# Optimization experiments

Measured on AMD Instinct MI355X. Metric: run time of the kernel, lower is better.

Reference implementation:

```python
import jax, jax.numpy as jnp
import numpy as np

N_NODES = 100000
N_EDGES = 6400000
IN_CH = 128
HID = 32
OUT = 16


def setup_inputs() -> dict:
    key = jax.random.key(0)
    k1, k2, k3, k4 = jax.random.split(key, 4)
    x = jax.random.normal(k1, (N_NODES, IN_CH), dtype=jnp.float32)
    edge_index = jax.random.randint(k2, (2, N_EDGES), 0, N_NODES, dtype=jnp.int64)
    # Glorot-style init like PyG GCNConv
    W1 = jax.random.normal(k3, (IN_CH, HID), dtype=jnp.float32) * (1.0 / np.sqrt(IN_CH))
    b1 = jnp.zeros((HID,), dtype=jnp.float32)
    W2 = jax.random.normal(k4, (HID, OUT), dtype=jnp.float32) * (1.0 / np.sqrt(HID))
    b2 = jnp.zeros((OUT,), dtype=jnp.float32)
    return {"x": x, "edge_index": edge_index, "W1": W1, "b1": b1, "W2": W2, "b2": b2}


def _gcn_layer(h, W, b, row, col, norm, n_nodes):
    # transform then propagate (PyG GCNConv order)
    m = h @ W                                   # [N, F_out]
    msg = m[row] * norm[:, None]                # gather + scale, [E+N, F_out]
    agg = jax.ops.segment_sum(msg, col, num_segments=n_nodes)
    return agg + b


def reference(x, edge_index, W1, b1, W2, b2):
    n = x.shape[0]
    loops = jnp.arange(n, dtype=edge_index.dtype)
    row = jnp.concatenate([edge_index[0], loops])  # source
    col = jnp.concatenate([edge_index[1], loops])  # target (aggregation index)
    # symmetric GCN normalization with self-loops; deg >= 1 always
    deg = jax.ops.segment_sum(jnp.ones_like(col, dtype=x.dtype), col, num_segments=n)
    deg_inv_sqrt = jax.lax.rsqrt(deg)
    norm = deg_inv_sqrt[row] * deg_inv_sqrt[col]
    h = jax.nn.relu(_gcn_layer(x, W1, b1, row, col, norm, n))
    # dropout p=0.5 is identity in eval mode
    return _gcn_layer(h, W2, b2, row, col, norm, n)
```

## Files before the change

### kernel.cpp

```cpp
#include <hip/hip_runtime.h>
#include <hip/hip_bf16.h>

#define IN_CH 128
#define HID 32
#define OUT_CH 16
#define NPW 128
#define NPW_SHIFT 7
#define NB_MAX 1024
#define FB_GRID 256
#define FB_THREADS 1024
#define CAP 12288
#define SCAN_CHUNK 1024
#define NXCD 8
#define EPT 8

typedef int vint4 __attribute__((ext_vector_type(4)));
typedef vint4 vint4u __attribute__((aligned(4)));

__global__ void detect_dtype(const void* ei, long long ecount, int n, int* flag) {
    int lane = threadIdx.x;
    const long long* p = (const long long*)ei;
    long long st = ecount / 64; if (st < 1) st = 1;
    long long idx = (long long)lane * st;
    bool ok = true;
    if (idx < ecount) {
        long long v = p[idx];
        ok = (v >= 0 && v < n);
    }
    unsigned long long mask = __ballot(ok);
    if (lane == 0) *flag = (mask == ~0ULL) ? 1 : 0;
}

__device__ __forceinline__ int load_idx(const void* ei, long long i, int is64) {
    return is64 ? (int)((const long long*)ei)[i] : ((const int*)ei)[i];
}

__device__ __forceinline__ void load_idx8_nt(const void* ei, long long off, int is64,
                                             int* c) {
    if (is64) {
        const long long* p = (const long long*)ei + off;
#pragma unroll
        for (int j = 0; j < 8; ++j) c[j] = (int)__builtin_nontemporal_load(p + j);
    } else {
        vint4 v0 = __builtin_nontemporal_load((const vint4*)((const int*)ei + off));
        vint4 v1 = __builtin_nontemporal_load((const vint4*)((const int*)ei + off + 4));
        c[0] = v0.x; c[1] = v0.y; c[2] = v0.z; c[3] = v0.w;
        c[4] = v1.x; c[5] = v1.y; c[6] = v1.z; c[7] = v1.w;
    }
}

__device__ __forceinline__ float bf_lo(unsigned int u) { return __uint_as_float(u << 16); }
__device__ __forceinline__ float bf_hi(unsigned int u) { return __uint_as_float(u & 0xFFFF0000u); }

__global__ __launch_bounds__(256) void zero_int(int* p, int n) {
    int i = blockIdx.x * 256 + threadIdx.x;
    if (i < n) p[i] = 0;
}

__global__ __launch_bounds__(256) void zero_float(float* p, long long n) {
    long long i = (long long)blockIdx.x * 256 + threadIdx.x;
    if (i < n) p[i] = 0.f;
}

__global__ __launch_bounds__(FB_THREADS) void bucket_hist(const void* ei, long long E,
                                                          const int* flag, int* bhist,
                                                          int nb, long long chunk) {
    __shared__ int hist[NB_MAX];
    for (int i = threadIdx.x; i < nb; i += FB_THREADS) hist[i] = 0;
    __syncthreads();
    long long lo = (long long)blockIdx.x * chunk;
    long long hi = lo + chunk; if (hi > E) hi = E;
    int is64 = *flag;
    if ((E & 7) == 0) {
        for (long long e = lo + (long long)threadIdx.x * EPT; e + EPT <= hi;
             e += (long long)FB_THREADS * EPT) {
            int c[8]; load_idx8_nt(ei, E + e, is64, c);
#pragma unroll
            for (int j = 0; j < 8; ++j) atomicAdd(&hist[c[j] >> NPW_SHIFT], 1);
        }
    } else {
        for (long long e = lo + threadIdx.x; e < hi; e += FB_THREADS)
            atomicAdd(&hist[load_idx(ei, E + e, is64) >> NPW_SHIFT], 1);
    }
    __syncthreads();
    for (int b = threadIdx.x; b < nb; b += FB_THREADS)
        bhist[b * FB_GRID + blockIdx.x] = hist[b];
}

__global__ __launch_bounds__(256) void scan_blocks(int* bhist, int* btot, int nb) {
    __shared__ int sd[FB_GRID];
    int b = blockIdx.x, t = threadIdx.x;
    int* p = bhist + (long long)b * FB_GRID;
    int v = p[t];
    sd[t] = v; __syncthreads();
    for (int off = 1; off < FB_GRID; off <<= 1) {
        int u = (t >= off) ? sd[t - off] : 0;
        __syncthreads(); sd[t] += u; __syncthreads();
    }
    p[t] = sd[t] - v;
    if (t == FB_GRID - 1) btot[b] = sd[t];
}

__global__ __launch_bounds__(1024) void scan_buckets(const int* btot, int* bstart, int nb) {
    __shared__ int sd[1024];
    int t = threadIdx.x;
    int a0 = (2 * t < nb) ? btot[2 * t] : 0;
    int a1 = (2 * t + 1 < nb) ? btot[2 * t + 1] : 0;
    sd[t] = a0 + a1; __syncthreads();
    for (int off = 1; off < 1024; off <<= 1) {
        int v = (t >= off) ? sd[t - off] : 0;
        __syncthreads(); sd[t] += v; __syncthreads();
    }
    int excl = sd[t] - (a0 + a1);
    if (2 * t < nb)     bstart[2 * t] = excl;
    if (2 * t + 1 < nb) bstart[2 * t + 1] = excl + a0;
    if (t == 1023) bstart[nb] = sd[t];
}

__global__ __launch_bounds__(FB_THREADS) void fill_bucket(const void* ei, long long E,
                                                          const int* flag,
                                                          const int* bhist,
                                                          const int* bstart,
                                                          int* bucketed, int nb,
                                                          long long chunk) {
    __shared__ int cur[NB_MAX];
    for (int b = threadIdx.x; b < nb; b += FB_THREADS)
        cur[b] = bstart[b] + bhist[b * FB_GRID + blockIdx.x];
    __syncthreads();
    long long lo = (long long)blockIdx.x * chunk;
    long long hi = lo + chunk; if (hi > E) hi = E;
    int is64 = *flag;
    if ((E & 7) == 0) {
        for (long long e = lo + (long long)threadIdx.x * EPT; e + EPT <= hi;
             e += (long long)FB_THREADS * EPT) {
            int c[8], r[8];
            load_idx8_nt(ei, E + e, is64, c);
            load_idx8_nt(ei, e, is64, r);
#pragma unroll
            for (int j = 0; j < 8; ++j) {
                int b = c[j] >> NPW_SHIFT;
                int pos = atomicAdd(&cur[b], 1);
                bucketed[pos] = r[j] | ((c[j] & (NPW - 1)) << 17);
            }
        }
    } else {
        for (long long e = lo + threadIdx.x; e < hi; e += FB_THREADS) {
            int col = load_idx(ei, E + e, is64);
            int row = load_idx(ei, e, is64);
            int b = col >> NPW_SHIFT;
            int pos = atomicAdd(&cur[b], 1);
            bucketed[pos] = row | ((col & (NPW - 1)) << 17);
        }
    }
}

__global__ __launch_bounds__(512) void csr_sort(const int* __restrict__ bucketed,
                                                const int* __restrict__ bstart,
                                                int* __restrict__ csr,
                                                int* __restrict__ offs,
                                                float* __restrict__ dinv,
                                                int nb, int n) {
    __shared__ int lds_e[CAP];
    __shared__ int hist[NPW];
    __shared__ int cur[NPW];
    int b = blockIdx.x, t = threadIdx.x;
    int s0 = bstart[b], s1 = bstart[b + 1];
    int cnt = s1 - s0;
    if (t < NPW) hist[t] = 0;
    __syncthreads();
    bool fit = (cnt <= CAP);
    int cnt4 = cnt & ~3;
    if (fit) {
        for (int i = t * 4; i < cnt4; i += 2048) {
            vint4u e4 = *(const vint4u*)(bucketed + s0 + i);
            lds_e[i + 0] = e4.x; atomicAdd(&hist[e4.x >> 17], 1);
            lds_e[i + 1] = e4.y; atomicAdd(&hist[e4.y >> 17], 1);
            lds_e[i + 2] = e4.z; atomicAdd(&hist[e4.z >> 17], 1);
            lds_e[i + 3] = e4.w; atomicAdd(&hist[e4.w >> 17], 1);
        }
        for (int i = cnt4 + t; i < cnt; i += 512) {
            int e = bucketed[s0 + i];
            lds_e[i] = e;
            atomicAdd(&hist[e >> 17], 1);
        }
    } else {
        for (int i = t * 4; i < cnt4; i += 2048) {
            vint4u e4 = *(const vint4u*)(bucketed + s0 + i);
            atomicAdd(&hist[e4.x >> 17], 1);
            atomicAdd(&hist[e4.y >> 17], 1);
            atomicAdd(&hist[e4.z >> 17], 1);
            atomicAdd(&hist[e4.w >> 17], 1);
        }
        for (int i = cnt4 + t; i < cnt; i += 512)
            atomicAdd(&hist[bucketed[s0 + i] >> 17], 1);
    }
    __syncthreads();
    if (t == 0) {
        int run = 0;
        for (int k = 0; k < NPW; ++k) { cur[k] = run; run += hist[k]; }
    }
    __syncthreads();
    if (t < NPW) {
        int node = b * NPW + t;
        if (node < n) {
            offs[node] = s0 + cur[t];
            dinv[node] = 1.0f / sqrtf((float)(hist[t] + 1));
        }
    }
    if (b == nb - 1 && t == 0) offs[n] = s1;
    __syncthreads();
    if (fit) {
        for (int i = t; i < cnt; i += 512) {
            int e = lds_e[i];
            int pos = atomicAdd(&cur[e >> 17], 1);
            csr[s0 + pos] = e & 0x1FFFF;
        }
    } else {
        for (int i = t; i < cnt; i += 512) {
            int e = bucketed[s0 + i];
            int pos = atomicAdd(&cur[e >> 17], 1);
            csr[s0 + pos] = e & 0x1FFFF;
        }
    }
}

template <int BF16>
__global__ __launch_bounds__(256) void gemm1p(const float* __restrict__ x,
                                              const float* __restrict__ W1,
                                              const float* __restrict__ dinv,
                                              float* __restrict__ m1f,
                                              __hip_bfloat16* __restrict__ m1b, int n) {
    __shared__ float sW[IN_CH * HID];
    __shared__ float sx[8][IN_CH];
    for (int i = threadIdx.x; i < IN_CH * HID; i += 256) sW[i] = W1[i];
    int g = threadIdx.x >> 5;
    int c = threadIdx.x & 31;
    long long node = (long long)blockIdx.x * 8 + g;
    bool active = node < n;
    if (active) {
        const float4* xr = (const float4*)(x + node * IN_CH);
        float4 v = xr[c];
        sx[g][c * 4 + 0] = v.x; sx[g][c * 4 + 1] = v.y;
        sx[g][c * 4 + 2] = v.z; sx[g][c * 4 + 3] = v.w;
    }
    __syncthreads();
    if (!active) return;
    float acc = 0.f;
#pragma unroll
    for (int k = 0; k < IN_CH; ++k)
        acc = fmaf(sx[g][k], sW[k * HID + c], acc);
    float v = acc * dinv[node];
    if (BF16) m1b[(node << 5) + c] = __float2bfloat16(v);
    else      m1f[(node << 5) + c] = v;
}

template <int BF16>
__global__ __launch_bounds__(256) void gemm2p(const float* __restrict__ h,
                                              const float* __restrict__ W2,
                                              const float* __restrict__ dinv,
                                              float* __restrict__ m2f,
                                              __hip_bfloat16* __restrict__ m2b, int n) {
    __shared__ float sW[HID * OUT_CH];
    for (int i = threadIdx.x; i < HID * OUT_CH; i += 256) sW[i] = W2[i];
    __syncthreads();
    long long t = (long long)blockIdx.x * 256 + threadIdx.x;
    long long node = t >> 4;
    int c = (int)(t & 15);
    if (node >= n) return;
    const float* hr = h + node * HID;
    float acc = 0.f;
#pragma unroll
    for (int k = 0; k < HID; ++k)
        acc = fmaf(hr[k], sW[k * OUT_CH + c], acc);
    float v = acc * dinv[node];
    if (BF16) m2b[(node << 4) + c] = __float2bfloat16(v);
    else      m2f[(node << 4) + c] = v;
}

__global__ __launch_bounds__(256) void agg1_bf(const unsigned int* __restrict__ m1b,
                                               const int* __restrict__ csr,
                                               const int* __restrict__ offs,
                                               const float* __restrict__ dinv,
                                               const float* __restrict__ b1,
                                               float* __restrict__ h, int n) {
    int g = threadIdx.x >> 4;
    int c = threadIdx.x & 15;
    long long node = (long long)blockIdx.x * 16 + g;
    if (node >= n) return;
    unsigned int us = m1b[(node << 4) + c];
    float accL = bf_lo(us), accH = bf_hi(us);
    int s = offs[node], e1 = offs[node + 1];
    for (; s + 7 < e1; s += 8) {
        vint4u a = *(const vint4u*)(csr + s);
        vint4u b = *(const vint4u*)(csr + s + 4);
        unsigned int u0 = m1b[((long long)a.x << 4) + c];
        unsigned int u1 = m1b[((long long)a.y << 4) + c];
        unsigned int u2 = m1b[((long long)a.z << 4) + c];
        unsigned int u3 = m1b[((long long)a.w << 4) + c];
        unsigned int u4 = m1b[((long long)b.x << 4) + c];
        unsigned int u5 = m1b[((long long)b.y << 4) + c];
        unsigned int u6 = m1b[((long long)b.z << 4) + c];
        unsigned int u7 = m1b[((long long)b.w << 4) + c];
        accL += bf_lo(u0); accH += bf_hi(u0);
        accL += bf_lo(u1); accH += bf_hi(u1);
        accL += bf_lo(u2); accH += bf_hi(u2);
        accL += bf_lo(u3); accH += bf_hi(u3);
        accL += bf_lo(u4); accH += bf_hi(u4);
        accL += bf_lo(u5); accH += bf_hi(u5);
        accL += bf_lo(u6); accH += bf_hi(u6);
        accL += bf_lo(u7); accH += bf_hi(u7);
    }
    for (; s < e1; ++s) {
        unsigned int u = m1b[((long long)csr[s] << 4) + c];
        accL += bf_lo(u); accH += bf_hi(u);
    }
    float di = dinv[node];
    float vL = accL * di + b1[2 * c];
    float vH = accH * di + b1[2 * c + 1];
    float2 val;
    val.x = vL > 0.f ? vL : 0.f;
    val.y = vH > 0.f ? vH : 0.f;
    *(float2*)(h + (node << 5) + 2 * c) = val;
}

__global__ __launch_bounds__(256) void agg2_bf(const unsigned int* __restrict__ m2b,
                                               const int* __restrict__ csr,
                                               const int* __restrict__ offs,
                                               const float* __restrict__ dinv,
                                               const float* __restrict__ b2,
                                               float* __restrict__ out, int n) {
    int g = threadIdx.x >> 3;
    int c = threadIdx.x & 7;
    long long node = (long long)blockIdx.x * 32 + g;
    if (node >= n) return;
    unsigned int us = m2b[(node << 3) + c];
    float accL = bf_lo(us), accH = bf_hi(us);
    int s = offs[node], e1 = offs[node + 1];
    for (; s + 7 < e1; s += 8) {
        vint4u a = *(const vint4u*)(csr + s);
        vint4u b = *(const vint4u*)(csr + s + 4);
        unsigned int u0 = m2b[((long long)a.x << 3) + c];
        unsigned int u1 = m2b[((long long)a.y << 3) + c];
        unsigned int u2 = m2b[((long long)a.z << 3) + c];
        unsigned int u3 = m2b[((long long)a.w << 3) + c];
        unsigned int u4 = m2b[((long long)b.x << 3) + c];
        unsigned int u5 = m2b[((long long)b.y << 3) + c];
        unsigned int u6 = m2b[((long long)b.z << 3) + c];
        unsigned int u7 = m2b[((long long)b.w << 3) + c];
        accL += bf_lo(u0); accH += bf_hi(u0);
        accL += bf_lo(u1); accH += bf_hi(u1);
        accL += bf_lo(u2); accH += bf_hi(u2);
        accL += bf_lo(u3); accH += bf_hi(u3);
        accL += bf_lo(u4); accH += bf_hi(u4);
        accL += bf_lo(u5); accH += bf_hi(u5);
        accL += bf_lo(u6); accH += bf_hi(u6);
        accL += bf_lo(u7); accH += bf_hi(u7);
    }
    for (; s < e1; ++s) {
        unsigned int u = m2b[((long long)csr[s] << 3) + c];
        accL += bf_lo(u); accH += bf_hi(u);
    }
    float di = dinv[node];
    float2 val;
    val.x = accL * di + b2[2 * c];
    val.y = accH * di + b2[2 * c + 1];
    *(float2*)(out + (node << 4) + 2 * c) = val;
}

__global__ __launch_bounds__(256) void count_edges(const void* ei, int* cnt,
                                                   long long E, const int* flag) {
    long long e0 = ((long long)blockIdx.x * 256 + threadIdx.x) * EPT;
    if (e0 >= E) return;
    int is64 = *flag;
    if (e0 + EPT <= E && (E & 7) == 0) {
        int c[EPT];
        load_idx8_nt(ei, E + e0, is64, c);
#pragma unroll
        for (int j = 0; j < EPT; ++j) atomicAdd(&cnt[c[j]], 1);
    } else {
        for (long long e = e0; e < E && e < e0 + EPT; ++e)
            atomicAdd(&cnt[load_idx(ei, E + e, is64)], 1);
    }
}

__global__ __launch_bounds__(256) void compute_dinv(const int* cnt, float* dinv, int n) {
    int i = blockIdx.x * 256 + threadIdx.x;
    if (i < n) dinv[i] = 1.0f / sqrtf((float)(cnt[i] + 1));
}

__global__ __launch_bounds__(256) void scan_partial(const int* cnt, int* partial, int n) {
    __shared__ int sd[256];
    int base = blockIdx.x * SCAN_CHUNK;
    int s = 0;
    for (int j = threadIdx.x; j < SCAN_CHUNK; j += 256) {
        int i = base + j;
        if (i < n) s += cnt[i];
    }
    sd[threadIdx.x] = s;
    __syncthreads();
    for (int off = 128; off > 0; off >>= 1) {
        if (threadIdx.x < off) sd[threadIdx.x] += sd[threadIdx.x + off];
        __syncthreads();
    }
    if (threadIdx.x == 0) partial[blockIdx.x] = sd[0];
}

__global__ void scan_serial(int* partial, int* offs, int nblk, int n) {
    if (threadIdx.x == 0 && blockIdx.x == 0) {
        int run = 0;
        for (int b = 0; b < nblk; ++b) { int t = partial[b]; partial[b] = run; run += t; }
        offs[n] = run;
    }
}

__global__ __launch_bounds__(256) void scan_final(const int* cnt, const int* partial,
                                                  int* offs, int n) {
    __shared__ int sd[256];
    int base = blockIdx.x * SCAN_CHUNK;
    int t = threadIdx.x;
    int loc[4]; int ts = 0;
#pragma unroll
    for (int j = 0; j < 4; ++j) {
        int i = base + t * 4 + j;
        loc[j] = (i < n) ? cnt[i] : 0;
        ts += loc[j];
    }
    sd[t] = ts;
    __syncthreads();
    for (int off = 1; off < 256; off <<= 1) {
        int v = (t >= off) ? sd[t - off] : 0;
        __syncthreads();
        sd[t] += v;
        __syncthreads();
    }
    int excl = sd[t] - ts + partial[blockIdx.x];
#pragma unroll
    for (int j = 0; j < 4; ++j) {
        int i = base + t * 4 + j;
        if (i < n) offs[i] = excl;
        excl += loc[j];
    }
}

__global__ __launch_bounds__(256) void copy_int(const int* src, int* dst, int n) {
    int i = blockIdx.x * 256 + threadIdx.x;
    if (i < n) dst[i] = src[i];
}

__global__ __launch_bounds__(256) void fill_csr_win(const void* ei, int* cursor, int* csr,
                                                    long long E, const int* flag,
                                                    int npw, int n) {
    int w = blockIdx.x & (NXCD - 1);
    int b = blockIdx.x >> 3;
    int lo = w * npw;
    int hi = lo + npw; if (hi > n) hi = n;
    long long e0 = ((long long)b * 256 + threadIdx.x) * EPT;
    if (e0 >= E) return;
    int is64 = *flag;
    if (e0 + EPT <= E && (E & 7) == 0) {
        int c[EPT];
        load_idx8_nt(ei, E + e0, is64, c);
#pragma unroll
        for (int j = 0; j < EPT; ++j) {
            if (c[j] >= lo && c[j] < hi) {
                int row = load_idx(ei, e0 + j, is64);
                int pos = atomicAdd(&cursor[c[j]], 1);
                csr[pos] = row;
            }
        }
    } else {
        for (long long e = e0; e < E && e < e0 + EPT; ++e) {
            int col = load_idx(ei, E + e, is64);
            if (col >= lo && col < hi) {
                int row = load_idx(ei, e, is64);
                int pos = atomicAdd(&cursor[col], 1);
                csr[pos] = row;
            }
        }
    }
}

__global__ __launch_bounds__(256) void scatter1(const float* __restrict__ m1s,
                                                const void* ei,
                                                float* __restrict__ h,
                                                long long E, const int* flag) {
    long long e = (long long)blockIdx.x * 8 + (threadIdx.x >> 5);
    int c = threadIdx.x & 31;
    if (e >= E) return;
    int is64 = *flag;
    int row = load_idx(ei, e, is64);
    int col = load_idx(ei, E + e, is64);
    atomicAdd(&h[(long long)col * HID + c], m1s[(long long)row * HID + c]);
}

__global__ __launch_bounds__(256) void fixup1(const float* __restrict__ m1s,
                                              const float* __restrict__ dinv,
                                              const float* __restrict__ b1,
                                              float* __restrict__ h, int n) {
    long long t = (long long)blockIdx.x * 256 + threadIdx.x;
    long long node = t >> 5; int c = (int)(t & 31);
    if (node >= n) return;
    float v = (h[node * HID + c] + m1s[node * HID + c]) * dinv[node] + b1[c];
    h[node * HID + c] = v > 0.f ? v : 0.f;
}

__global__ __launch_bounds__(256) void scatter2(const float* __restrict__ m2s,
                                                const void* ei,
                                                float* __restrict__ out,
                                                long long E, const int* flag) {
    long long e = (long long)blockIdx.x * 16 + (threadIdx.x >> 4);
    int c = threadIdx.x & 15;
    if (e >= E) return;
    int is64 = *flag;
    int row = load_idx(ei, e, is64);
    int col = load_idx(ei, E + e, is64);
    atomicAdd(&out[(long long)col * OUT_CH + c], m2s[(long long)row * OUT_CH + c]);
}

__global__ __launch_bounds__(256) void fixup2(const float* __restrict__ m2s,
                                              const float* __restrict__ dinv,
                                              const float* __restrict__ b2,
                                              float* __restrict__ out, int n) {
    long long t = (long long)blockIdx.x * 256 + threadIdx.x;
    long long node = t >> 4; int c = (int)(t & 15);
    if (node >= n) return;
    out[node * OUT_CH + c] = (out[node * OUT_CH + c] + m2s[node * OUT_CH + c]) * dinv[node] + b2[c];
}

extern "C" void kernel_launch(void* const* d_in, const int* in_sizes, int n_in,
                              void* d_out, int out_size, void* d_ws, size_t ws_size,
                              hipStream_t stream) {
    const float* x  = (const float*)d_in[0];
    const void*  ei = d_in[1];
    const float* W1 = (const float*)d_in[2];
    const float* b1 = (const float*)d_in[3];
    const float* W2 = (const float*)d_in[4];
    const float* b2 = (const float*)d_in[5];
    float* out = (float*)d_out;

    const int n = in_sizes[0] / IN_CH;
    const long long E = in_sizes[1] / 2;
    const int nb = (n + NPW - 1) / NPW;

    char* w = (char*)d_ws;
    size_t used = 0;
    auto carve = [&](size_t bytes) -> void* {
        void* p = (void*)(w + used);
        used += (bytes + 255) & ~(size_t)255;
        return p;
    };
    auto A = [](size_t b) -> size_t { return (b + 255) & ~(size_t)255; };

    int*   bstart  = (int*)carve((size_t)(NB_MAX + 1) * 4);
    int*   btot    = (int*)carve((size_t)NB_MAX * 4);
    float* dinv    = (float*)carve((size_t)n * 4);
    int*   flag    = (int*)carve(256);
    int*   offs    = (int*)carve((size_t)(n + 1) * 4);
    int*   cnt     = (int*)carve((size_t)n * 4);
    int*   partial = (int*)carve(4096);
    const size_t base = used;

    const size_t bhistB = A((size_t)nb * FB_GRID * 4);
    const size_t mbB    = A((size_t)n * HID * 2);
    const size_t hB     = A((size_t)n * HID * 4);
    const size_t needT1 = base + bhistB + 2 * A((size_t)E * 4) + mbB + hB;
    const size_t needT2 = base + A((size_t)E * 4) + mbB + hB;
    const size_t needT3 = base + 2 * A((size_t)n * HID * 4);
    const bool tier1 = (ws_size >= needT1) && (n <= 131071) && (nb <= NB_MAX);
    const bool tier2 = !tier1 && (ws_size >= needT2) && (n <= 131071);

    const int nblkN  = (n + 255) / 256;
    const int nblkEv = (int)((E + 256LL * EPT - 1) / (256LL * EPT));
    const int nblkSc = (n + SCAN_CHUNK - 1) / SCAN_CHUNK;
    const int nblkH  = (int)(((long long)n * HID + 255) / 256);
    const int nblkO  = (int)(((long long)n * OUT_CH + 255) / 256);

    detect_dtype<<<1, 64, 0, stream>>>(ei, E, n, flag);

    if (tier1) {
        int*   bhist    = (int*)carve((size_t)nb * FB_GRID * 4);
        int*   bucketed = (int*)carve((size_t)E * 4);
        int*   csr      = (int*)carve((size_t)E * 4);
        __hip_bfloat16* m1b = (__hip_bfloat16*)carve((size_t)n * HID * 2);
        float* h  = (float*)carve((size_t)n * HID * 4);
        __hip_bfloat16* m2b = m1b;

        const long long chunk = (((E + FB_GRID - 1) / FB_GRID) + 7) & ~7LL;

        bucket_hist<<<FB_GRID, FB_THREADS, 0, stream>>>(ei, E, flag, bhist, nb, chunk);
        scan_blocks<<<nb, FB_GRID, 0, stream>>>(bhist, btot, nb);
        scan_buckets<<<1, 1024, 0, stream>>>(btot, bstart, nb);
        fill_bucket<<<FB_GRID, FB_THREADS, 0, stream>>>(ei, E, flag, bhist, bstart,
                                                        bucketed, nb, chunk);
        csr_sort<<<nb, 512, 0, stream>>>(bucketed, bstart, csr, offs, dinv, nb, n);

        gemm1p<1><<<(n + 7) / 8, 256, 0, stream>>>(x, W1, dinv, nullptr, m1b, n);
        agg1_bf<<<(n + 15) / 16, 256, 0, stream>>>((const unsigned int*)m1b, csr, offs,
                                                   dinv, b1, h, n);
        gemm2p<1><<<nblkO, 256, 0, stream>>>(h, W2, dinv, nullptr, m2b, n);
        agg2_bf<<<(n + 31) / 32, 256, 0, stream>>>((const unsigned int*)m2b, csr, offs,
                                                   dinv, b2, out, n);
    } else if (tier2) {
        int*   csr = (int*)carve((size_t)E * 4);
        __hip_bfloat16* m1b = (__hip_bfloat16*)carve((size_t)n * HID * 2);
        float* h  = (float*)carve((size_t)n * HID * 4);
        __hip_bfloat16* m2b = m1b;

        zero_int<<<nblkN, 256, 0, stream>>>(cnt, n);
        count_edges<<<nblkEv, 256, 0, stream>>>(ei, cnt, E, flag);
        compute_dinv<<<nblkN, 256, 0, stream>>>(cnt, dinv, n);
        scan_partial<<<nblkSc, 256, 0, stream>>>(cnt, partial, n);
        scan_serial<<<1, 64, 0, stream>>>(partial, offs, nblkSc, n);
        scan_final<<<nblkSc, 256, 0, stream>>>(cnt, partial, offs, n);
        copy_int<<<nblkN, 256, 0, stream>>>(offs, cnt, n);

        const int npw2 = (n + NXCD - 1) / NXCD;
        fill_csr_win<<<nblkEv * NXCD, 256, 0, stream>>>(ei, cnt, csr, E, flag, npw2, n);

        gemm1p<1><<<(n + 7) / 8, 256, 0, stream>>>(x, W1, dinv, nullptr, m1b, n);
        agg1_bf<<<(n + 15) / 16, 256, 0, stream>>>((const unsigned int*)m1b, csr, offs,
                                                   dinv, b1, h, n);
        gemm2p<1><<<nblkO, 256, 0, stream>>>(h, W2, dinv, nullptr, m2b, n);
        agg2_bf<<<(n + 31) / 32, 256, 0, stream>>>((const unsigned int*)m2b, csr, offs,
                                                   dinv, b2, out, n);
    } else if (ws_size >= needT3) {
        float* m1 = (float*)carve((size_t)n * HID * 4);
        float* h  = (float*)carve((size_t)n * HID * 4);
        float* m2 = m1;

        zero_int<<<nblkN, 256, 0, stream>>>(cnt, n);
        count_edges<<<nblkEv, 256, 0, stream>>>(ei, cnt, E, flag);
        compute_dinv<<<nblkN, 256, 0, stream>>>(cnt, dinv, n);

        gemm1p<0><<<(n + 7) / 8, 256, 0, stream>>>(x, W1, dinv, m1, nullptr, n);
        zero_float<<<nblkH, 256, 0, stream>>>(h, (long long)n * HID);
        scatter1<<<(int)((E + 7) / 8), 256, 0, stream>>>(m1, ei, h, E, flag);
        fixup1<<<nblkH, 256, 0, stream>>>(m1, dinv, b1, h, n);
        gemm2p<0><<<nblkO, 256, 0, stream>>>(h, W2, dinv, m2, nullptr, n);
        zero_float<<<nblkO, 256, 0, stream>>>(out, (long long)n * OUT_CH);
        scatter2<<<(int)((E + 15) / 16), 256, 0, stream>>>(m2, ei, out, E, flag);
        fixup2<<<nblkO, 256, 0, stream>>>(m2, dinv, b2, out, n);
    }
}
```

Measured before the change: 305.4 us.

## Stage bucket scatter in LDS per block and write contiguous runs

The bucket fill kernel now builds a local histogram and prefix sum per block, scatters edges into shared memory sorted by bucket, then copies each bucket's run contiguously to global memory. This replaces random per-edge global scatter writes with coalesced run writes. The grid is also changed to 512 blocks of 512 threads, with scan_blocks generalized to handle that grid width. The cost is an extra histogram pass over the column indices inside the fill kernel, plus a large LDS footprint that may limit occupancy.

```diff
diff --git a/kernel.cpp b/kernel.cpp
--- a/kernel.cpp
+++ b/kernel.cpp
@@ -7,8 +7,8 @@
 #define NPW 128
 #define NPW_SHIFT 7
 #define NB_MAX 1024
-#define FB_GRID 256
-#define FB_THREADS 1024
+#define CAPF 12800
+#define FBT 512
 #define CAP 12288
 #define SCAN_CHUNK 1024
 #define NXCD 8
@@ -62,43 +62,51 @@
     if (i < n) p[i] = 0.f;
 }
 
-__global__ __launch_bounds__(FB_THREADS) void bucket_hist(const void* ei, long long E,
-                                                          const int* flag, int* bhist,
-                                                          int nb, long long chunk) {
+__global__ __launch_bounds__(FBT) void bucket_hist(const void* ei, long long E,
+                                                   const int* flag, int* bhist,
+                                                   int nb, long long chunk, int fbgrid) {
     __shared__ int hist[NB_MAX];
-    for (int i = threadIdx.x; i < nb; i += FB_THREADS) hist[i] = 0;
+    for (int i = threadIdx.x; i < nb; i += FBT) hist[i] = 0;
     __syncthreads();
     long long lo = (long long)blockIdx.x * chunk;
     long long hi = lo + chunk; if (hi > E) hi = E;
     int is64 = *flag;
     if ((E & 7) == 0) {
         for (long long e = lo + (long long)threadIdx.x * EPT; e + EPT <= hi;
-             e += (long long)FB_THREADS * EPT) {
+             e += (long long)FBT * EPT) {
             int c[8]; load_idx8_nt(ei, E + e, is64, c);
 #pragma unroll
             for (int j = 0; j < 8; ++j) atomicAdd(&hist[c[j] >> NPW_SHIFT], 1);
         }
     } else {
-        for (long long e = lo + threadIdx.x; e < hi; e += FB_THREADS)
+        for (long long e = lo + threadIdx.x; e < hi; e += FBT)
             atomicAdd(&hist[load_idx(ei, E + e, is64) >> NPW_SHIFT], 1);
     }
     __syncthreads();
-    for (int b = threadIdx.x; b < nb; b += FB_THREADS)
-        bhist[b * FB_GRID + blockIdx.x] = hist[b];
-}
-
-__global__ __launch_bounds__(256) void scan_blocks(int* bhist, int* btot, int nb) {
-    __shared__ int sd[FB_GRID];
+    for (int b = threadIdx.x; b < nb; b += FBT)
+        bhist[(long long)b * fbgrid + blockIdx.x] = hist[b];
+}
+
+__global__ __launch_bounds__(256) void scan_blocks(int* bhist, int* btot, int nb,
+                                                   int fbgrid) {
+    __shared__ int sd[256];
     int b = blockIdx.x, t = threadIdx.x;
-    int* p = bhist + (long long)b * FB_GRID;
-    int v = p[t];
-    sd[t] = v; __syncthreads();
-    for (int off = 1; off < FB_GRID; off <<= 1) {
-        int u = (t >= off) ? sd[t - off] : 0;
-        __syncthreads(); sd[t] += u; __syncthreads();
-    }
-    p[t] = sd[t] - v;
-    if (t == FB_GRID - 1) btot[b] = sd[t];
+    int* p = bhist + (long long)b * fbgrid;
+    int running = 0;
+    for (int j0 = 0; j0 < fbgrid; j0 += 256) {
+        int j = j0 + t;
+        int v = (j < fbgrid) ? p[j] : 0;
+        sd[t] = v; __syncthreads();
+        for (int off = 1; off < 256; off <<= 1) {
+            int u = (t >= off) ? sd[t - off] : 0;
+            __syncthreads(); sd[t] += u; __syncthreads();
+        }
+        if (j < fbgrid) p[j] = running + sd[t] - v;
+        int tot = sd[255];
+        __syncthreads();
+        running += tot;
+    }
+    if (t == 0) btot[b] = running;
 }
 
 __global__ __launch_bounds__(1024) void scan_buckets(const int* btot, int* bstart, int nb) {
@@ -117,39 +125,91 @@
     if (t == 1023) bstart[nb] = sd[t];
 }
 
-__global__ __launch_bounds__(FB_THREADS) void fill_bucket(const void* ei, long long E,
-                                                          const int* flag,
-                                                          const int* bhist,
-                                                          const int* bstart,
-                                                          int* bucketed, int nb,
-                                                          long long chunk) {
+__global__ __launch_bounds__(FBT) void fill_sort(const void* ei, long long E,
+                                                 const int* flag, const int* bhist,
+                                                 const int* bstart, int* bucketed,
+                                                 int nb, long long chunk, int fbgrid) {
+    __shared__ int lds[CAPF];
+    __shared__ int hist[NB_MAX];
+    __shared__ int base[NB_MAX];
     __shared__ int cur[NB_MAX];
-    for (int b = threadIdx.x; b < nb; b += FB_THREADS)
-        cur[b] = bstart[b] + bhist[b * FB_GRID + blockIdx.x];
-    __syncthreads();
-    long long lo = (long long)blockIdx.x * chunk;
+    int blk = blockIdx.x, t = threadIdx.x;
+    long long lo = (long long)blk * chunk;
     long long hi = lo + chunk; if (hi > E) hi = E;
+    int cnt = (int)(hi - lo);
+    for (int i = t; i < nb; i += FBT) hist[i] = 0;
+    __syncthreads();
     int is64 = *flag;
-    if ((E & 7) == 0) {
-        for (long long e = lo + (long long)threadIdx.x * EPT; e + EPT <= hi;
-             e += (long long)FB_THREADS * EPT) {
-            int c[8], r[8];
-            load_idx8_nt(ei, E + e, is64, c);
-            load_idx8_nt(ei, e, is64, r);
-#pragma unroll
-            for (int j = 0; j < 8; ++j) {
-                int b = c[j] >> NPW_SHIFT;
-                int pos = atomicAdd(&cur[b], 1);
-                bucketed[pos] = r[j] | ((c[j] & (NPW - 1)) << 17);
+    bool vec = ((E & 7) == 0) && ((chunk & 7) == 0);
+
+    if (vec) {
+        for (long long e = lo + (long long)t * EPT; e + EPT <= hi; e += (long long)FBT * EPT) {
+            int c[8]; load_idx8_nt(ei, E + e, is64, c);
+#pragma unroll
+            for (int j = 0; j < 8; ++j) atomicAdd(&hist[c[j] >> NPW_SHIFT], 1);
+        }
+    } else {
+        for (long long e = lo + t; e < hi; e += FBT)
+            atomicAdd(&hist[load_idx(ei, E + e, is64) >> NPW_SHIFT], 1);
+    }
+    __syncthreads();
+
+    if (cnt <= CAPF) {
+        int a0 = (2 * t < nb) ? hist[2 * t] : 0;
+        int a1 = (2 * t + 1 < nb) ? hist[2 * t + 1] : 0;
+        base[t] = a0 + a1; __syncthreads();
+        for (int off = 1; off < FBT; off <<= 1) {
+            int u = (t >= off) ? base[t - off] : 0;
+            __syncthreads(); base[t] += u; __syncthreads();
+        }
+        int incl = base[t];
+        __syncthreads();
+        int excl = incl - (a0 + a1);
+        if (2 * t < nb)     { base[2 * t] = excl;          cur[2 * t] = excl; }
+        if (2 * t + 1 < nb) { base[2 * t + 1] = excl + a0; cur[2 * t + 1] = excl + a0; }
+        __syncthreads();
+
+        if (vec) {
+            for (long long e = lo + (long long)t * EPT; e + EPT <= hi; e += (long long)FBT * EPT) {
+                int c[8], r[8];
+                load_idx8_nt(ei, E + e, is64, c);
+                load_idx8_nt(ei, e, is64, r);
+#pragma unroll
+                for (int j = 0; j < 8; ++j) {
+                    int b = c[j] >> NPW_SHIFT;
+                    int p = atomicAdd(&cur[b], 1);
+                    lds[p] = r[j] | ((c[j] & (NPW - 1)) << 17);
+                }
             }
+        } else {
+            for (long long e = lo + t; e < hi; e += FBT) {
+                int col = load_idx(ei, E + e, is64);
+                int row = load_idx(ei, e, is64);
+                int b = col >> NPW_SHIFT;
+                int p = atomicAdd(&cur[b], 1);
+                lds[p] = row | ((col & (NPW - 1)) << 17);
+            }
+        }
+        __syncthreads();
+
+        int grp = t >> 4, lane = t & 15;
+        for (int b = grp; b < nb; b += 32) {
+            int l0 = base[b], c0 = hist[b];
+            if (!c0) continue;
+            int g0 = bstart[b] + bhist[(long long)b * fbgrid + blk];
+            for (int j = lane; j < c0; j += 16)
+                bucketed[g0 + j] = lds[l0 + j];
         }
     } else {
-        for (long long e = lo + threadIdx.x; e < hi; e += FB_THREADS) {
+        for (int b = t; b < nb; b += FBT)
+            cur[b] = bstart[b] + bhist[(long long)b * fbgrid + blk];
+        __syncthreads();
+        for (long long e = lo + t; e < hi; e += FBT) {
             int col = load_idx(ei, E + e, is64);
             int row = load_idx(ei, e, is64);
             int b = col >> NPW_SHIFT;
-            int pos = atomicAdd(&cur[b], 1);
-            bucketed[pos] = row | ((col & (NPW - 1)) << 17);
+            int p = atomicAdd(&cur[b], 1);
+            bucketed[p] = row | ((col & (NPW - 1)) << 17);
         }
     }
 }
@@ -542,6 +602,9 @@
     const long long E = in_sizes[1] / 2;
     const int nb = (n + NPW - 1) / NPW;
 
+    const long long chunkF = (((E + 511) / 512) + 7) & ~7LL;
+    const int fbgrid = (int)((E + chunkF - 1) / chunkF);
+
     char* w = (char*)d_ws;
     size_t used = 0;
     auto carve = [&](size_t bytes) -> void* {
@@ -560,13 +623,14 @@
     int*   partial = (int*)carve(4096);
     const size_t base = used;
 
-    const size_t bhistB = A((size_t)nb * FB_GRID * 4);
+    const size_t bhistB = A((size_t)nb * fbgrid * 4);
     const size_t mbB    = A((size_t)n * HID * 2);
     const size_t hB     = A((size_t)n * HID * 4);
     const size_t needT1 = base + bhistB + 2 * A((size_t)E * 4) + mbB + hB;
     const size_t needT2 = base + A((size_t)E * 4) + mbB + hB;
     const size_t needT3 = base + 2 * A((size_t)n * HID * 4);
-    const bool tier1 = (ws_size >= needT1) && (n <= 131071) && (nb <= NB_MAX);
+    const bool tier1 = (ws_size >= needT1) && (n <= 131071) && (nb <= NB_MAX) &&
+                       (chunkF <= CAPF || true);
     const bool tier2 = !tier1 && (ws_size >= needT2) && (n <= 131071);
 
     const int nblkN  = (n + 255) / 256;
@@ -578,20 +642,18 @@
     detect_dtype<<<1, 64, 0, stream>>>(ei, E, n, flag);
 
     if (tier1) {
-        int*   bhist    = (int*)carve((size_t)nb * FB_GRID * 4);
+        int*   bhist    = (int*)carve((size_t)nb * fbgrid * 4);
         int*   bucketed = (int*)carve((size_t)E * 4);
         int*   csr      = (int*)carve((size_t)E * 4);
         __hip_bfloat16* m1b = (__hip_bfloat16*)carve((size_t)n * HID * 2);
         float* h  = (float*)carve((size_t)n * HID * 4);
         __hip_bfloat16* m2b = m1b;
 
-        const long long chunk = (((E + FB_GRID - 1) / FB_GRID) + 7) & ~7LL;
-
-        bucket_hist<<<FB_GRID, FB_THREADS, 0, stream>>>(ei, E, flag, bhist, nb, chunk);
-        scan_blocks<<<nb, FB_GRID, 0, stream>>>(bhist, btot, nb);
+        bucket_hist<<<fbgrid, FBT, 0, stream>>>(ei, E, flag, bhist, nb, chunkF, fbgrid);
+        scan_blocks<<<nb, 256, 0, stream>>>(bhist, btot, nb, fbgrid);
         scan_buckets<<<1, 1024, 0, stream>>>(btot, bstart, nb);
-        fill_bucket<<<FB_GRID, FB_THREADS, 0, stream>>>(ei, E, flag, bhist, bstart,
-                                                        bucketed, nb, chunk);
+        fill_sort<<<fbgrid, FBT, 0, stream>>>(ei, E, flag, bhist, bstart,
+                                              bucketed, nb, chunkF, fbgrid);
         csr_sort<<<nb, 512, 0, stream>>>(bucketed, bstart, csr, offs, dinv, nb, n);
 
         gemm1p<1><<<(n + 7) / 8, 256, 0, stream>>>(x, W1, dinv, nullptr, m1b, n);
```

New measurement: 263.8 us. 1.16x faster.
